# Optimization experiments

Measured on AMD Instinct MI355X. Metric: run time of the kernel, lower is better.

## Reference

```python
import jax, jax.numpy as jnp
import numpy as np


def setup_inputs() -> dict:
    key = jax.random.key(0)
    ks = jax.random.split(key, 8)
    B, L, F, H, A = 128, 196, 2048, 512, 512
    features = jax.random.normal(ks[0], (B, L, F), dtype=jnp.float32)
    hidden_state = jax.random.normal(ks[1], (B, H), dtype=jnp.float32)
    # Linear params (PyTorch layout: weight [out, in], bias [out]); scaled like kaiming-uniform
    W_enc = jax.random.normal(ks[2], (A, F), dtype=jnp.float32) / np.sqrt(F)
    b_enc = jnp.zeros((A,), dtype=jnp.float32)
    W_dec = jax.random.normal(ks[3], (A, H), dtype=jnp.float32) / np.sqrt(H)
    b_dec = jnp.zeros((A,), dtype=jnp.float32)
    W_com = jax.random.normal(ks[4], (1, A), dtype=jnp.float32) / np.sqrt(A)
    b_com = jnp.zeros((1,), dtype=jnp.float32)
    return {
        "features": features, "hidden_state": hidden_state,
        "W_enc": W_enc, "b_enc": b_enc,
        "W_dec": W_dec, "b_dec": b_dec,
        "W_com": W_com, "b_com": b_com,
    }


def reference(features, hidden_state, W_enc, b_enc, W_dec, b_dec, W_com, b_com):
    # encoder_context: [B, L, A]
    enc = jnp.einsum('blf,af->bla', features, W_enc) + b_enc
    # decoder_context: [B, 1, A]
    dec = (hidden_state @ W_dec.T + b_dec)[:, None, :]
    # relu + linear to scalar score (dropout in eval mode = identity): [B, L]
    scores = jnp.einsum('bla,a->bl', jax.nn.relu(enc + dec), W_com[0]) + b_com[0]
    alpha = jax.nn.softmax(scores, axis=1)  # [B, L]
    weighted_features = jnp.einsum('blf,bl->bf', features, alpha)  # [B, F]
    return weighted_features, alpha
```

## Files before the change

kernel.cpp:

```cpp
#include <hip/hip_runtime.h>
#include <hip/hip_bf16.h>
#include <math.h>

#define B_  128
#define L_  196
#define F_  2048
#define H_  512
#define A_  512
#define ML_ (B_*L_)

typedef _Float16 half8 __attribute__((ext_vector_type(8)));
typedef _Float16 half4v __attribute__((ext_vector_type(4)));
typedef _Float16 half2v __attribute__((ext_vector_type(2)));
typedef float f32x4 __attribute__((ext_vector_type(4)));

__device__ __forceinline__ void gld_lds16(const void* g, void* l) {
  __builtin_amdgcn_global_load_lds((const __attribute__((address_space(1))) void*)g,
                                   (__attribute__((address_space(3))) void*)l, 16, 0, 0);
}

__global__ __launch_bounds__(256) void k_prep(const float4* __restrict__ Wenc4,
                                              half4v* __restrict__ wH,
                                              const float* __restrict__ hs,
                                              const float* __restrict__ Wdec,
                                              const float* __restrict__ bdec,
                                              const float* __restrict__ benc,
                                              float* __restrict__ dec,
                                              float* __restrict__ scores) {
  const int b = blockIdx.x, t = threadIdx.x;

  {
    const int base = b * 2048 + t;
    float4 v[8];
#pragma unroll
    for (int j = 0; j < 8; j++) v[j] = Wenc4[base + j * 256];
#pragma unroll
    for (int j = 0; j < 8; j++) {
      half4v o = { (_Float16)v[j].x, (_Float16)v[j].y, (_Float16)v[j].z, (_Float16)v[j].w };
      wH[base + j * 256] = o;
    }
  }

  const int g = b * 256 + t;
  if (g < ML_) scores[g] = 0.f;

  __shared__ float h[H_];
  h[t]       = hs[b * H_ + t];
  h[t + 256] = hs[b * H_ + t + 256];
  __syncthreads();

#pragma unroll
  for (int r = 0; r < 2; r++) {
    const int a = t + r * 256;
    float acc = bdec[a] + benc[a];
    const float4* wr = (const float4*)(Wdec + (size_t)a * H_);
#pragma unroll 4
    for (int k4 = 0; k4 < H_ / 4; k4++) {
      const float4 w = wr[k4];
      acc += w.x * h[4*k4] + w.y * h[4*k4+1] + w.z * h[4*k4+2] + w.w * h[4*k4+3];
    }
    dec[b * A_ + a] = acc;
  }
}

__global__ __launch_bounds__(256) void k_scores_mfma(const float* __restrict__ fA,
                                                     const _Float16* __restrict__ fB,
                                                     const float* __restrict__ dec,
                                                     const float* __restrict__ wcom,
                                                     float* __restrict__ scores) {
  __shared__ float     As[128 * 64];
  __shared__ _Float16  Bs[128 * 64];
  __shared__ float decS[2][128];

  const int tid  = threadIdx.x;
  const int lane = tid & 63;
  const int w    = tid >> 6;

  const int l = blockIdx.x;
  int at_, mt;
  if (l < 768) { at_ = (l >> 3) & 3; mt = (l >> 5) * 8 + (l & 7); }
  else { const int idx = l - 768; at_ = idx >> 2; mt = 192 + (idx & 3); }
  const int a0 = at_ * 128;
  const int m0 = mt * 128;

  const int wm   = w & 1;
  const int wn   = w >> 1;
  const int quad = lane >> 4;
  const int l16  = lane & 15;

  f32x4 acc[4][4];
#pragma unroll
  for (int i = 0; i < 4; i++)
#pragma unroll
    for (int j = 0; j < 4; j++)
#pragma unroll
      for (int k = 0; k < 4; k++) acc[i][j][k] = 0.f;

  const int b0 = m0 / L_;
  {
    const int i = tid >> 7;
    const int j = tid & 127;
    int bb = b0 + i; if (bb > B_ - 1) bb = B_ - 1;
    decS[i][j] = dec[bb * A_ + a0 + j];
  }

  const int srowA = lane >> 4;
  const float* pA0;
  const float* pA1;
  {
    const size_t rbase = (size_t)(m0 + w * 32 + srowA) * F_;
    pA0 = fA + rbase + (size_t)(((lane & 15) ^ srowA) * 4);
    pA1 = fA + rbase + (size_t)(((lane & 15) ^ srowA ^ 4) * 4);
  }
  const int srowB = lane >> 3;
  const _Float16* pB = fB + (size_t)(a0 + w * 32 + srowB) * F_
                          + (size_t)(((lane & 7) ^ srowB) * 8);

  for (int kt = 0; kt < F_; kt += 64) {
#pragma unroll
    for (int i = 0; i < 8; i++)
      gld_lds16(((i & 1) ? pA1 : pA0) + (size_t)(i * 4) * F_ + kt,
                &As[(w * 32 + i * 4) * 64]);
#pragma unroll
    for (int i = 0; i < 4; i++)
      gld_lds16(pB + (size_t)(i * 8) * F_ + kt,
                &Bs[(w * 32 + i * 8) * 64]);
    __syncthreads();

#pragma unroll
    for (int kk = 0; kk < 2; kk++) {
      half8 af[4], bf[4];
#pragma unroll
      for (int mf = 0; mf < 4; mf++) {
        const int row = wm * 64 + mf * 16 + l16;
        const int g0  = kk * 8 + quad * 2;
        const int s0  = g0 ^ (row & 7);
        const int s1  = s0 ^ 1;
        const float4 f0 = *(const float4*)&As[row * 64 + s0 * 4];
        const float4 f1 = *(const float4*)&As[row * 64 + s1 * 4];
        union { half8 v8; half2v h2[4]; } u;
        u.h2[0] = (half2v)__builtin_amdgcn_cvt_pkrtz(f0.x, f0.y);
        u.h2[1] = (half2v)__builtin_amdgcn_cvt_pkrtz(f0.z, f0.w);
        u.h2[2] = (half2v)__builtin_amdgcn_cvt_pkrtz(f1.x, f1.y);
        u.h2[3] = (half2v)__builtin_amdgcn_cvt_pkrtz(f1.z, f1.w);
        af[mf] = u.v8;
      }
#pragma unroll
      for (int at = 0; at < 4; at++) {
        const int row = wn * 64 + at * 16 + l16;
        const int s   = (kk * 4 + quad) ^ (row & 7);
        bf[at] = *(const half8*)&Bs[row * 64 + s * 8];
      }
#pragma unroll
      for (int mf = 0; mf < 4; mf++)
#pragma unroll
        for (int at = 0; at < 4; at++)
          acc[mf][at] = __builtin_amdgcn_mfma_f32_16x16x32_f16(af[mf], bf[at], acc[mf][at], 0, 0, 0);
    }
    __syncthreads();
  }

  float w4[4];
#pragma unroll
  for (int at = 0; at < 4; at++) w4[at] = wcom[a0 + wn * 64 + at * 16 + l16];

#pragma unroll
  for (int mf = 0; mf < 4; mf++) {
#pragma unroll
    for (int r = 0; r < 4; r++) {
      const int m  = m0 + wm * 64 + mf * 16 + quad * 4 + r;
      const int db = m / L_ - b0;
      float p = 0.f;
#pragma unroll
      for (int at = 0; at < 4; at++) {
        const float e = acc[mf][at][r] + decS[db][wn * 64 + at * 16 + l16];
        p = fmaf(fmaxf(e, 0.f), w4[at], p);
      }
      p += __shfl_xor(p, 1);
      p += __shfl_xor(p, 2);
      p += __shfl_xor(p, 4);
      p += __shfl_xor(p, 8);
      if (l16 == 0) atomicAdd(&scores[m], p);
    }
  }
}

__global__ __launch_bounds__(256) void k_attn_f32(const float* __restrict__ feat,
                                                  const float* __restrict__ scores,
                                                  float* __restrict__ alpha,
                                                  float* __restrict__ out) {
  const int fc = blockIdx.x, b = blockIdx.y, t = threadIdx.x;
  __shared__ float al[L_];
  __shared__ float redm[4];
  __shared__ float reds[4];

  float s = (t < L_) ? scores[b * L_ + t] : -INFINITY;
  float m = s;
#pragma unroll
  for (int o = 32; o >= 1; o >>= 1) m = fmaxf(m, __shfl_xor(m, o));
  if ((t & 63) == 0) redm[t >> 6] = m;
  __syncthreads();
  m = fmaxf(fmaxf(redm[0], redm[1]), fmaxf(redm[2], redm[3]));
  float e = (t < L_) ? expf(s - m) : 0.f;
  float sum = e;
#pragma unroll
  for (int o = 32; o >= 1; o >>= 1) sum += __shfl_xor(sum, o);
  if ((t & 63) == 0) reds[t >> 6] = sum;
  __syncthreads();
  sum = reds[0] + reds[1] + reds[2] + reds[3];
  if (t < L_) {
    const float a = e / sum;
    al[t] = a;
    if (fc == 0) alpha[b * L_ + t] = a;
  }
  __syncthreads();

  const int f0 = fc * 512 + t * 2;
  const float2* fp = (const float2*)(feat + (size_t)b * L_ * F_ + f0);
  float ax = 0.f, ay = 0.f;
#pragma unroll 4
  for (int ll = 0; ll < L_; ll++) {
    const float2 v = fp[(size_t)ll * (F_ / 2)];
    const float wgt = al[ll];
    ax = fmaf(v.x, wgt, ax);
    ay = fmaf(v.y, wgt, ay);
  }
  float2 o = { ax, ay };
  *(float2*)(out + (size_t)b * F_ + f0) = o;
}

__global__ __launch_bounds__(256) void k_scores_f32(const float* __restrict__ feat,
                                                    const float* __restrict__ Wenc,
                                                    const float* __restrict__ dec,
                                                    const float* __restrict__ wcom,
                                                    float* __restrict__ scores) {
  __shared__ float As[16][128];
  __shared__ float Bs[16][128];
  const int tid = threadIdx.x;
  const int m0 = blockIdx.x * 128;
  const int a0 = blockIdx.y * 128;
  const int tx = tid & 15;
  const int ty = tid >> 4;
  float acc[8][8];
#pragma unroll
  for (int i = 0; i < 8; i++)
#pragma unroll
    for (int j = 0; j < 8; j++) acc[i][j] = 0.f;
  for (int kt = 0; kt < F_; kt += 16) {
#pragma unroll
    for (int rep = 0; rep < 2; rep++) {
      const int idx = rep * 256 + tid;
      const int row = idx >> 2;
      const int kp  = (idx & 3) << 2;
      const float4 v = *(const float4*)(feat + (size_t)(m0 + row) * F_ + kt + kp);
      As[kp+0][row] = v.x; As[kp+1][row] = v.y; As[kp+2][row] = v.z; As[kp+3][row] = v.w;
      const float4 w = *(const float4*)(Wenc + (size_t)(a0 + row) * F_ + kt + kp);
      Bs[kp+0][row] = w.x; Bs[kp+1][row] = w.y; Bs[kp+2][row] = w.z; Bs[kp+3][row] = w.w;
    }
    __syncthreads();
#pragma unroll
    for (int k = 0; k < 16; k++) {
      float ar[8], br[8];
      *(float4*)&ar[0] = *(const float4*)&As[k][ty * 8];
      *(float4*)&ar[4] = *(const float4*)&As[k][ty * 8 + 4];
      *(float4*)&br[0] = *(const float4*)&Bs[k][tx * 8];
      *(float4*)&br[4] = *(const float4*)&Bs[k][tx * 8 + 4];
#pragma unroll
      for (int i = 0; i < 8; i++)
#pragma unroll
        for (int j = 0; j < 8; j++) acc[i][j] = fmaf(ar[i], br[j], acc[i][j]);
    }
    __syncthreads();
  }
  float w8[8];
  *(float4*)&w8[0] = *(const float4*)(wcom + a0 + tx * 8);
  *(float4*)&w8[4] = *(const float4*)(wcom + a0 + tx * 8 + 4);
#pragma unroll
  for (int i = 0; i < 8; i++) {
    const int m = m0 + ty * 8 + i;
    const int b = m / L_;
    const float* dp = dec + b * A_ + a0 + tx * 8;
    float p = 0.f;
#pragma unroll
    for (int j = 0; j < 8; j++) {
      const float e = acc[i][j] + dp[j];
      p = fmaf(fmaxf(e, 0.f), w8[j], p);
    }
    p += __shfl_xor(p, 1);
    p += __shfl_xor(p, 2);
    p += __shfl_xor(p, 4);
    p += __shfl_xor(p, 8);
    if (tx == 0) atomicAdd(&scores[m], p);
  }
}

__global__ __launch_bounds__(256) void k_dec_only(const float* __restrict__ hs,
                                                  const float* __restrict__ Wdec,
                                                  const float* __restrict__ bdec,
                                                  const float* __restrict__ benc,
                                                  float* __restrict__ dec,
                                                  float* __restrict__ scores) {
  const int b = blockIdx.x, t = threadIdx.x;
  const int g = b * 256 + t;
  if (g < ML_) scores[g] = 0.f;
  __shared__ float h[H_];
  h[t]       = hs[b * H_ + t];
  h[t + 256] = hs[b * H_ + t + 256];
  __syncthreads();
#pragma unroll
  for (int r = 0; r < 2; r++) {
    const int a = t + r * 256;
    float acc = bdec[a] + benc[a];
    const float4* wr = (const float4*)(Wdec + (size_t)a * H_);
#pragma unroll 4
    for (int k4 = 0; k4 < H_ / 4; k4++) {
      const float4 w = wr[k4];
      acc += w.x * h[4*k4] + w.y * h[4*k4+1] + w.z * h[4*k4+2] + w.w * h[4*k4+3];
    }
    dec[b * A_ + a] = acc;
  }
}

extern "C" void kernel_launch(void* const* d_in, const int* in_sizes, int n_in,
                              void* d_out, int out_size, void* d_ws, size_t ws_size,
                              hipStream_t stream) {
  const float* feat = (const float*)d_in[0];
  const float* hs   = (const float*)d_in[1];
  const float* Wenc = (const float*)d_in[2];
  const float* benc = (const float*)d_in[3];
  const float* Wdec = (const float*)d_in[4];
  const float* bdec = (const float*)d_in[5];
  const float* wcom = (const float*)d_in[6];

  float* out   = (float*)d_out;
  float* alpha = out + B_ * F_;
  float* dec    = (float*)d_ws;
  float* scores = dec + B_ * A_;

  const size_t need = (size_t)(B_ * A_ + ML_) * 4 + (size_t)A_ * F_ * 2;

  if (ws_size >= need) {
    _Float16* wH = (_Float16*)(scores + ML_);
    k_prep<<<dim3(128), dim3(256), 0, stream>>>(
        (const float4*)Wenc, (half4v*)wH, hs, Wdec, bdec, benc, dec, scores);
    k_scores_mfma<<<dim3(784), dim3(256), 0, stream>>>(feat, wH, dec, wcom, scores);
  } else {
    k_dec_only<<<dim3(B_), dim3(256), 0, stream>>>(hs, Wdec, bdec, benc, dec, scores);
    k_scores_f32<<<dim3(ML_ / 128, A_ / 128), dim3(256), 0, stream>>>(feat, Wenc, dec, wcom, scores);
  }
  k_attn_f32<<<dim3(4, B_), dim3(256), 0, stream>>>(feat, scores, alpha, out);
}
```

Measured before the change: 423.9 us.

## Convert A tile to fp16 before LDS with register prefetch; split softmax from weighted sum

The scores GEMM no longer copies fp32 features straight into LDS. Each thread now loads its fp32 slice into registers one K-step ahead, converts it to fp16, and stores a swizzled fp16 tile. This halves LDS footprint and read traffic and removes the repeated per-fragment conversions in the MFMA loop, at the cost of more registers and no direct global-to-LDS path for A. Softmax moves into its own kernel, and the weighted-sum kernel now uses 128-thread blocks over 8 feature chunks with two independent accumulator chains, which adds a launch but raises block count and memory-level parallelism.

```diff
diff --git a/kernel.cpp b/kernel.cpp
--- a/kernel.cpp
+++ b/kernel.cpp
@@ -68,7 +68,7 @@
                                                      const float* __restrict__ dec,
                                                      const float* __restrict__ wcom,
                                                      float* __restrict__ scores) {
-  __shared__ float     As[128 * 64];
+  __shared__ _Float16  As[128 * 64];
   __shared__ _Float16  Bs[128 * 64];
   __shared__ float decS[2][128];
 
@@ -104,28 +104,39 @@
     decS[i][j] = dec[bb * A_ + a0 + j];
   }
 
-  const int srowA = lane >> 4;
-  const float* pA0;
-  const float* pA1;
-  {
-    const size_t rbase = (size_t)(m0 + w * 32 + srowA) * F_;
-    pA0 = fA + rbase + (size_t)(((lane & 15) ^ srowA) * 4);
-    pA1 = fA + rbase + (size_t)(((lane & 15) ^ srowA ^ 4) * 4);
-  }
+  const int arow = tid >> 1;
+  const int ah   = tid & 1;
+  const int ar7  = arow & 7;
+  const float* aP = fA + (size_t)(m0 + arow) * F_ + ah * 32;
   const int srowB = lane >> 3;
   const _Float16* pB = fB + (size_t)(a0 + w * 32 + srowB) * F_
                           + (size_t)(((lane & 7) ^ srowB) * 8);
 
+  float4 fr[8];
+#pragma unroll
+  for (int jj = 0; jj < 8; jj++) fr[jj] = *(const float4*)(aP + jj * 4);
+
   for (int kt = 0; kt < F_; kt += 64) {
 #pragma unroll
-    for (int i = 0; i < 8; i++)
-      gld_lds16(((i & 1) ? pA1 : pA0) + (size_t)(i * 4) * F_ + kt,
-                &As[(w * 32 + i * 4) * 64]);
-#pragma unroll
     for (int i = 0; i < 4; i++)
-      gld_lds16(pB + (size_t)(i * 8) * F_ + kt,
-                &Bs[(w * 32 + i * 8) * 64]);
+      gld_lds16(pB + (size_t)(i * 8) * F_ + kt, &Bs[(w * 32 + i * 8) * 64]);
+
+#pragma unroll
+    for (int j = 0; j < 4; j++) {
+      union { half8 v; half2v h2[4]; } u;
+      u.h2[0] = (half2v)__builtin_amdgcn_cvt_pkrtz(fr[2*j].x,   fr[2*j].y);
+      u.h2[1] = (half2v)__builtin_amdgcn_cvt_pkrtz(fr[2*j].z,   fr[2*j].w);
+      u.h2[2] = (half2v)__builtin_amdgcn_cvt_pkrtz(fr[2*j+1].x, fr[2*j+1].y);
+      u.h2[3] = (half2v)__builtin_amdgcn_cvt_pkrtz(fr[2*j+1].z, fr[2*j+1].w);
+      *(half8*)&As[arow * 64 + (((ah << 2) | j) ^ ar7) * 8] = u.v;
+    }
     __syncthreads();
+
+    if (kt + 64 < F_) {
+#pragma unroll
+      for (int jj = 0; jj < 8; jj++)
+        fr[jj] = *(const float4*)(aP + kt + 64 + jj * 4);
+    }
 
 #pragma unroll
     for (int kk = 0; kk < 2; kk++) {
@@ -133,23 +144,12 @@
 #pragma unroll
       for (int mf = 0; mf < 4; mf++) {
         const int row = wm * 64 + mf * 16 + l16;
-        const int g0  = kk * 8 + quad * 2;
-        const int s0  = g0 ^ (row & 7);
-        const int s1  = s0 ^ 1;
-        const float4 f0 = *(const float4*)&As[row * 64 + s0 * 4];
-        const float4 f1 = *(const float4*)&As[row * 64 + s1 * 4];
-        union { half8 v8; half2v h2[4]; } u;
-        u.h2[0] = (half2v)__builtin_amdgcn_cvt_pkrtz(f0.x, f0.y);
-        u.h2[1] = (half2v)__builtin_amdgcn_cvt_pkrtz(f0.z, f0.w);
-        u.h2[2] = (half2v)__builtin_amdgcn_cvt_pkrtz(f1.x, f1.y);
-        u.h2[3] = (half2v)__builtin_amdgcn_cvt_pkrtz(f1.z, f1.w);
-        af[mf] = u.v8;
+        af[mf] = *(const half8*)&As[row * 64 + ((((kk << 2) | quad)) ^ (row & 7)) * 8];
       }
 #pragma unroll
       for (int at = 0; at < 4; at++) {
         const int row = wn * 64 + at * 16 + l16;
-        const int s   = (kk * 4 + quad) ^ (row & 7);
-        bf[at] = *(const half8*)&Bs[row * 64 + s * 8];
+        bf[at] = *(const half8*)&Bs[row * 64 + ((((kk << 2) | quad)) ^ (row & 7)) * 8];
       }
 #pragma unroll
       for (int mf = 0; mf < 4; mf++)
@@ -185,47 +185,54 @@
   }
 }
 
-__global__ __launch_bounds__(256) void k_attn_f32(const float* __restrict__ feat,
-                                                  const float* __restrict__ scores,
-                                                  float* __restrict__ alpha,
+__global__ __launch_bounds__(256) void k_softmax(const float* __restrict__ scores,
+                                                 float* __restrict__ alpha) {
+  const int b = blockIdx.x, t = threadIdx.x;
+  __shared__ float redm[4];
+  __shared__ float reds[4];
+
+  float s = (t < L_) ? scores[b * L_ + t] : -INFINITY;
+  float m = s;
+#pragma unroll
+  for (int o = 32; o >= 1; o >>= 1) m = fmaxf(m, __shfl_xor(m, o));
+  if ((t & 63) == 0) redm[t >> 6] = m;
+  __syncthreads();
+  m = fmaxf(fmaxf(redm[0], redm[1]), fmaxf(redm[2], redm[3]));
+  float e = (t < L_) ? expf(s - m) : 0.f;
+  float sum = e;
+#pragma unroll
+  for (int o = 32; o >= 1; o >>= 1) sum += __shfl_xor(sum, o);
+  if ((t & 63) == 0) reds[t >> 6] = sum;
+  __syncthreads();
+  sum = reds[0] + reds[1] + reds[2] + reds[3];
+  if (t < L_) alpha[b * L_ + t] = e / sum;
+}
+
+__global__ __launch_bounds__(128) void k_attn_f32(const float* __restrict__ feat,
+                                                  const float* __restrict__ alpha,
                                                   float* __restrict__ out) {
   const int fc = blockIdx.x, b = blockIdx.y, t = threadIdx.x;
   __shared__ float al[L_];
-  __shared__ float redm[4];
-  __shared__ float reds[4];
-
-  float s = (t < L_) ? scores[b * L_ + t] : -INFINITY;
-  float m = s;
-#pragma unroll
-  for (int o = 32; o >= 1; o >>= 1) m = fmaxf(m, __shfl_xor(m, o));
-  if ((t & 63) == 0) redm[t >> 6] = m;
-  __syncthreads();
-  m = fmaxf(fmaxf(redm[0], redm[1]), fmaxf(redm[2], redm[3]));
-  float e = (t < L_) ? expf(s - m) : 0.f;
-  float sum = e;
-#pragma unroll
-  for (int o = 32; o >= 1; o >>= 1) sum += __shfl_xor(sum, o);
-  if ((t & 63) == 0) reds[t >> 6] = sum;
-  __syncthreads();
-  sum = reds[0] + reds[1] + reds[2] + reds[3];
-  if (t < L_) {
-    const float a = e / sum;
-    al[t] = a;
-    if (fc == 0) alpha[b * L_ + t] = a;
-  }
-  __syncthreads();
-
-  const int f0 = fc * 512 + t * 2;
+
+  al[t] = alpha[b * L_ + t];
+  if (t < L_ - 128) al[t + 128] = alpha[b * L_ + t + 128];
+  __syncthreads();
+
+  const int f0 = fc * 256 + t * 2;
   const float2* fp = (const float2*)(feat + (size_t)b * L_ * F_ + f0);
-  float ax = 0.f, ay = 0.f;
-#pragma unroll 4
-  for (int ll = 0; ll < L_; ll++) {
-    const float2 v = fp[(size_t)ll * (F_ / 2)];
-    const float wgt = al[ll];
-    ax = fmaf(v.x, wgt, ax);
-    ay = fmaf(v.y, wgt, ay);
-  }
-  float2 o = { ax, ay };
+  float a0x = 0.f, a0y = 0.f, a1x = 0.f, a1y = 0.f;
+#pragma unroll 7
+  for (int ll = 0; ll < 98; ll++) {
+    const float2 v0 = fp[(size_t)ll * (F_ / 2)];
+    const float2 v1 = fp[(size_t)(ll + 98) * (F_ / 2)];
+    const float w0 = al[ll];
+    const float w1 = al[ll + 98];
+    a0x = fmaf(v0.x, w0, a0x);
+    a0y = fmaf(v0.y, w0, a0y);
+    a1x = fmaf(v1.x, w1, a1x);
+    a1y = fmaf(v1.y, w1, a1y);
+  }
+  float2 o = { a0x + a1x, a0y + a1y };
   *(float2*)(out + (size_t)b * F_ + f0) = o;
 }
 
@@ -348,5 +355,6 @@
     k_dec_only<<<dim3(B_), dim3(256), 0, stream>>>(hs, Wdec, bdec, benc, dec, scores);
     k_scores_f32<<<dim3(ML_ / 128, A_ / 128), dim3(256), 0, stream>>>(feat, Wenc, dec, wcom, scores);
   }
-  k_attn_f32<<<dim3(4, B_), dim3(256), 0, stream>>>(feat, scores, alpha, out);
-}
+  k_softmax<<<dim3(B_), dim3(256), 0, stream>>>(scores, alpha);
+  k_attn_f32<<<dim3(8, B_), dim3(128), 0, stream>>>(feat, alpha, out);
+}
```

Result: slower. 472.1 us (+11.4%).
